# Kernel tuning notes

Hardware: AMD Instinct MI355X
Metric: run time of the kernel (lower is better)

## Reference

```python
import jax, jax.numpy as jnp
import numpy as np

QUERY_BREADTH = 50


def setup_inputs() -> dict:
    key = jax.random.key(0)
    k1, k2, k3 = jax.random.split(key, 3)
    B, D_K, D_V, M = 8192, 128, 128, 32768
    return {
        "queries": jax.random.normal(k1, (B, D_K), dtype=jnp.float32),
        "keys": jax.random.normal(k2, (M, D_K), dtype=jnp.float32),
        "values": jax.random.normal(k3, (M, D_V), dtype=jnp.float32),
    }


def reference(queries, keys, values):
    # [B, M] dense similarity (dot-product) lookup
    lookup = jnp.einsum("bd,md->bm", queries, keys)
    # top-k over memory slots
    top_ks, top_k_inds = jax.lax.top_k(lookup, QUERY_BREADTH)  # [B, K]
    weights = jax.nn.softmax(top_ks, axis=1)                   # [B, K]
    # gather value rows and weighted-sum: [B, K, D_V] -> [B, D_V]
    selected_values = values[top_k_inds]
    weighted_selection = jnp.einsum("bkd,bk->bd", selected_values, weights)
    return (weighted_selection, top_k_inds, weights)
```

## Files before the change

### kernel.cpp

```cpp
#include <hip/hip_runtime.h>
#include <hip/hip_bf16.h>

constexpr int D    = 128;
constexpr int KSEL = 50;
constexpr int CAP  = 256;
constexpr int CNT_STRIDE = 16;
constexpr int HT_PER_BLK = 16;
constexpr int SLOTS = 24;
constexpr float THR_SIGMA = 2.6f;

typedef __attribute__((ext_vector_type(8))) short bf16x8;
typedef __attribute__((ext_vector_type(4))) float f32x4;

__device__ inline unsigned short f32_to_bf16_rne(float f) {
    unsigned u = __float_as_uint(f);
    unsigned r = 0x7FFFu + ((u >> 16) & 1u);
    return (unsigned short)((u + r) >> 16);
}

#define GLOAD_LDS16(gp, lp) \
  __builtin_amdgcn_global_load_lds((const __attribute__((address_space(1))) void*)(gp), \
                                   (__attribute__((address_space(3))) void*)(lp), 16, 0, 0)

__global__ void k_convert(const float* __restrict__ src,
                          unsigned short* __restrict__ dst, int nrows) {
    int gid = blockIdx.x * 256 + threadIdx.x;
    if (gid >= nrows * 32) return;
    int r  = gid >> 5;
    int d4 = (gid & 31) << 2;
    const float4 v = *(const float4*)(src + (size_t)r * D + d4);
    ushort4 o;
    o.x = f32_to_bf16_rne(v.x);
    o.y = f32_to_bf16_rne(v.y);
    o.z = f32_to_bf16_rne(v.z);
    o.w = f32_to_bf16_rne(v.w);
    size_t base = (size_t)(r >> 6) * 8192 + (size_t)(d4 >> 3) * 512
                + (size_t)(r & 63) * 8 + (d4 & 7);
    *(ushort4*)(dst + base) = o;
}

__global__ void k0_norm(const float* __restrict__ Q, float* __restrict__ tq) {
    const int q = blockIdx.x;
    const int lane = threadIdx.x;
    float v0 = Q[(size_t)q * D + lane];
    float v1 = Q[(size_t)q * D + 64 + lane];
    float ss = v0 * v0 + v1 * v1;
    #pragma unroll
    for (int off = 32; off > 0; off >>= 1)
        ss += __shfl_xor(ss, off);
    if (lane == 0) tq[q] = THR_SIGMA * sqrtf(ss);
}

__global__ __launch_bounds__(256, 3) void k1_mfma_filter(
    const unsigned short* __restrict__ Qb, const unsigned short* __restrict__ Kb,
    const float* __restrict__ tq, int* __restrict__ cnt,
    unsigned* __restrict__ ckey)
{
    __shared__ unsigned short Ks[2][8192];
    __shared__ unsigned cand[128][SLOTS];
    __shared__ int lcnt[128];

    const int tid  = threadIdx.x;
    const int wid  = tid >> 6;
    const int lane = tid & 63;
    const int qb   = blockIdx.x;
    const int ch   = blockIdx.y;

    if (tid < 128) lcnt[tid] = 0;

    const int wq  = wid >> 1;
    const int wk  = wid & 1;
    const int fr  = lane & 15;
    const int dgl = lane >> 4;

    const unsigned short* gkc = Kb + (size_t)ch * (HT_PER_BLK * 8192);
    #pragma unroll
    for (int i = 0; i < 4; ++i) {
        int inst = wid * 4 + i;
        GLOAD_LDS16(gkc + inst * 512 + lane * 8, &Ks[0][inst * 512]);
    }

    bf16x8 qf[4][4];
    {
        const unsigned short* qbase_p = Qb + (size_t)(qb * 2 + wq) * 8192;
        #pragma unroll
        for (int ks = 0; ks < 4; ++ks)
            #pragma unroll
            for (int fi = 0; fi < 4; ++fi)
                qf[ks][fi] = *(const bf16x8*)(qbase_p + (ks * 4 + dgl) * 512
                                              + (fi * 16 + fr) * 8);
    }

    const int qbase = qb * 128 + wq * 64;
    const int crow  = (lane >> 4) * 4;
    const int ccol  = lane & 15;

    float thr[4][4];
    #pragma unroll
    for (int fi = 0; fi < 4; ++fi)
        #pragma unroll
        for (int r = 0; r < 4; ++r)
            thr[fi][r] = tq[qbase + fi * 16 + crow + r];

    __syncthreads();

    for (int t = 0; t < HT_PER_BLK; ++t) {
        const int cur = t & 1;

        if (t + 1 < HT_PER_BLK) {
            const unsigned short* gt = gkc + (size_t)(t + 1) * 8192;
            #pragma unroll
            for (int i = 0; i < 4; ++i) {
                int inst = wid * 4 + i;
                GLOAD_LDS16(gt + inst * 512 + lane * 8, &Ks[cur ^ 1][inst * 512]);
            }
        }
        __builtin_amdgcn_sched_barrier(0);

        f32x4 acc[4][2];
        const f32x4 fzero = {0.f, 0.f, 0.f, 0.f};
        #pragma unroll
        for (int i = 0; i < 4; ++i) {
            acc[i][0] = fzero; acc[i][1] = fzero;
        }

        #pragma unroll
        for (int ks = 0; ks < 4; ++ks) {
            const int dg = ks * 4 + dgl;
            bf16x8 b[2];
            #pragma unroll
            for (int fj = 0; fj < 2; ++fj)
                b[fj] = *(const bf16x8*)&Ks[cur][dg * 512
                                                + (wk * 32 + fj * 16 + fr) * 8];
            #pragma unroll
            for (int fi = 0; fi < 4; ++fi)
                #pragma unroll
                for (int fj = 0; fj < 2; ++fj)
                    acc[fi][fj] = __builtin_amdgcn_mfma_f32_16x16x32_bf16(
                        qf[ks][fi], b[fj], acc[fi][fj], 0, 0, 0);
        }

        const int kbase = (ch * HT_PER_BLK + t) * 64 + wk * 32;
        #pragma unroll
        for (int fi = 0; fi < 4; ++fi) {
            #pragma unroll
            for (int r = 0; r < 4; ++r) {
                unsigned m = 0;
                #pragma unroll
                for (int fj = 0; fj < 2; ++fj)
                    if (acc[fi][fj][r] > thr[fi][r]) m |= (1u << fj);
                if (m) {
                    const int ql = wq * 64 + fi * 16 + crow + r;
                    int p = atomicAdd(&lcnt[ql], __popc(m));
                    #pragma unroll
                    for (int fj = 0; fj < 2; ++fj) {
                        if ((m >> fj) & 1u) {
                            const int key = kbase + fj * 16 + ccol;
                            const unsigned pk =
                                ((unsigned)f32_to_bf16_rne(acc[fi][fj][r]) << 15)
                                | (unsigned)(0x7FFF - key);
                            if (p < SLOTS) cand[ql][p] = pk;
                            ++p;
                        }
                    }
                }
            }
        }
        __syncthreads();
    }

    if (tid < 128) {
        const int q = qb * 128 + tid;
        int n = lcnt[tid]; if (n > SLOTS) n = SLOTS;
        if (n > 0) {
            int base = atomicAdd(&cnt[(size_t)q * CNT_STRIDE], n);
            for (int i = 0; i < n; ++i) {
                int p = base + i;
                if (p < CAP) ckey[(size_t)q * CAP + p] = cand[tid][i];
            }
        }
    }
}

__global__ __launch_bounds__(256) void k2_select(
    const float* __restrict__ Q, const float* __restrict__ Kmat,
    const float* __restrict__ V,
    const unsigned* __restrict__ ckey, const int* __restrict__ cnt, int M,
    float* __restrict__ outW, float* __restrict__ outI, float* __restrict__ outP)
{
    const int lane = threadIdx.x & 63;
    const int wid  = threadIdx.x >> 6;
    const int q    = blockIdx.x * 4 + wid;

    __shared__ float Qrow[4][D];
    Qrow[wid][lane]      = Q[(size_t)q * D + lane];
    Qrow[wid][lane + 64] = Q[(size_t)q * D + lane + 64];
    __syncthreads();

    int n = cnt[(size_t)q * CNT_STRIDE]; if (n > CAP) n = CAP;

    unsigned key[4];
    #pragma unroll
    for (int s = 0; s < 4; ++s) {
        int pos = s * 64 + lane;
        key[s] = (pos < n) ? ckey[(size_t)q * CAP + pos] : 0u;
    }

    #pragma unroll
    for (int k = 2; k <= 256; k <<= 1) {
        #pragma unroll
        for (int j = k >> 1; j > 0; j >>= 1) {
            if (j >= 64) {
                const int jr = j >> 6;
                #pragma unroll
                for (int r = 0; r < 4; ++r) {
                    if ((r & jr) == 0) {
                        const int r2 = r | jr;
                        const bool up = (((r << 6) & k) == 0);
                        const bool sw = up ? (key[r2] > key[r]) : (key[r2] < key[r]);
                        if (sw) { unsigned tmp = key[r]; key[r] = key[r2]; key[r2] = tmp; }
                    }
                }
            } else {
                #pragma unroll
                for (int r = 0; r < 4; ++r) {
                    unsigned other = __shfl_xor(key[r], j);
                    const bool up = ((((r << 6) | lane) & k) == 0);
                    const bool hi = (lane & j) != 0;
                    const bool oBetter = other > key[r];
                    const bool keepOther = (up != hi) ? oBetter : !oBetter;
                    if (keepOther) key[r] = other;
                }
            }
        }
    }

    const unsigned key0 = key[0];
    const int id0 = key0 ? (0x7FFF - (int)(key0 & 0x7FFFu)) : 0x7FFFFFFF;

    float sv;
    {
        const float* kr = Kmat + (size_t)(key0 ? id0 : 0) * D;
        float a = 0.f;
        #pragma unroll 8
        for (int d0 = 0; d0 < D; d0 += 4) {
            float4 kv = *(const float4*)(kr + d0);
            a = fmaf(Qrow[wid][d0 + 0], kv.x, a);
            a = fmaf(Qrow[wid][d0 + 1], kv.y, a);
            a = fmaf(Qrow[wid][d0 + 2], kv.z, a);
            a = fmaf(Qrow[wid][d0 + 3], kv.w, a);
        }
        sv = key0 ? a : -__builtin_inff();
    }

    unsigned long long fk = key0
        ? (((unsigned long long)__float_as_uint(sv) << 32)
           | (unsigned long long)(0xFFFFFFFFu - (unsigned)id0))
        : 0ull;
    #pragma unroll
    for (int k = 2; k <= 64; k <<= 1) {
        #pragma unroll
        for (int j = k >> 1; j > 0; j >>= 1) {
            unsigned long long other = __shfl_xor(fk, j);
            const bool up = ((lane & k) == 0) || (k == 64);
            const bool hi = (lane & j) != 0;
            const bool oBetter = other > fk;
            const bool keepOther = (up != hi) ? oBetter : !oBetter;
            if (keepOther) fk = other;
        }
    }
    float svf = __uint_as_float((unsigned)(fk >> 32));
    int   si  = (int)(0xFFFFFFFFu - (unsigned)(fk & 0xFFFFFFFFull));

    float m0 = __shfl(svf, 0);
    float e = (lane < KSEL) ? (float)exp((double)svf - (double)m0) : 0.f;
    float sum = e;
    #pragma unroll
    for (int off = 32; off > 0; off >>= 1) sum += __shfl_xor(sum, off);
    float w = e / sum;

    if (lane < KSEL) {
        outI[(size_t)q * KSEL + lane] = (float)si;
        outP[(size_t)q * KSEL + lane] = w;
    }

    float g0 = 0.f, g1 = 0.f;
    for (int cc = 0; cc < KSEL; ++cc) {
        int   idc = __shfl(si, cc);
        float wc  = __shfl(w,  cc);
        if ((unsigned)idc >= (unsigned)M) idc = 0;
        const float2 vv = *(const float2*)(V + (size_t)idc * D + lane * 2);
        g0 = fmaf(wc, vv.x, g0);
        g1 = fmaf(wc, vv.y, g1);
    }
    float2 res; res.x = g0; res.y = g1;
    *(float2*)(outW + (size_t)q * D + lane * 2) = res;
}

extern "C" void kernel_launch(void* const* d_in, const int* in_sizes, int n_in,
                              void* d_out, int out_size, void* d_ws, size_t ws_size,
                              hipStream_t stream) {
    const float* Q  = (const float*)d_in[0];
    const float* Km = (const float*)d_in[1];
    const float* V  = (const float*)d_in[2];

    const int B = in_sizes[0] / D;
    const int M = in_sizes[1] / D;

    float* out  = (float*)d_out;
    float* outW = out;
    float* outI = out + (size_t)B * D;
    float* outP = outI + (size_t)B * KSEL;

    char* ws = (char*)d_ws;
    float*          tq   = (float*)ws;
    int*            cnt  = (int*)(ws + (size_t)B * 4);
    unsigned*       ckey = (unsigned*)(ws + (size_t)B * 4 + (size_t)B * CNT_STRIDE * 4);
    unsigned short* Qb   = (unsigned short*)((char*)ckey + (size_t)B * CAP * 4);
    unsigned short* Kb   = (unsigned short*)((char*)Qb + (size_t)B * D * 2);

    hipMemsetAsync(cnt, 0, (size_t)B * CNT_STRIDE * 4, stream);
    k_convert<<<(B * 32 + 255) / 256, 256, 0, stream>>>(Q,  Qb, B);
    k_convert<<<(M * 32 + 255) / 256, 256, 0, stream>>>(Km, Kb, M);
    k0_norm<<<B, 64, 0, stream>>>(Q, tq);
    dim3 g1(B / 128, M / (64 * HT_PER_BLK));
    k1_mfma_filter<<<g1, 256, 0, stream>>>(Qb, Kb, tq, cnt, ckey);
    k2_select<<<B / 4, 256, 0, stream>>>(Q, Km, V, ckey, cnt, M, outW, outI, outP);
}
```

Measured before the change: 202.4 us.

## Load key tiles straight to registers and fuse query norm into conversion

The filter kernel no longer stages key tiles through double-buffered LDS with async global-to-LDS loads. Each wave now reads its B fragments directly from global memory (L2-cached), which removes the per-tile barrier and the 32KB LDS buffer. The query-norm threshold is computed inside the bf16 conversion kernel, so the separate norm launch goes away, and the occupancy hint in launch bounds is dropped. The trade-off is that every wave issues redundant global loads for the same keys, with no software prefetch to hide latency.

```diff
diff --git a/kernel.cpp b/kernel.cpp
--- a/kernel.cpp
+++ b/kernel.cpp
@@ -5,7 +5,7 @@
 constexpr int KSEL = 50;
 constexpr int CAP  = 256;
 constexpr int CNT_STRIDE = 16;
-constexpr int HT_PER_BLK = 16;
+constexpr int GRP_PER_BLK = 16;
 constexpr int SLOTS = 24;
 constexpr float THR_SIGMA = 2.6f;
 
@@ -18,17 +18,21 @@
     return (unsigned short)((u + r) >> 16);
 }
 
-#define GLOAD_LDS16(gp, lp) \
-  __builtin_amdgcn_global_load_lds((const __attribute__((address_space(1))) void*)(gp), \
-                                   (__attribute__((address_space(3))) void*)(lp), 16, 0, 0)
-
 __global__ void k_convert(const float* __restrict__ src,
-                          unsigned short* __restrict__ dst, int nrows) {
+                          unsigned short* __restrict__ dst, int nrows,
+                          float* __restrict__ tq) {
     int gid = blockIdx.x * 256 + threadIdx.x;
     if (gid >= nrows * 32) return;
     int r  = gid >> 5;
     int d4 = (gid & 31) << 2;
     const float4 v = *(const float4*)(src + (size_t)r * D + d4);
+    if (tq) {
+        float ss = v.x * v.x + v.y * v.y + v.z * v.z + v.w * v.w;
+        #pragma unroll
+        for (int off = 16; off > 0; off >>= 1)
+            ss += __shfl_xor(ss, off);
+        if ((gid & 31) == 0) tq[r] = THR_SIGMA * sqrtf(ss);
+    }
     ushort4 o;
     o.x = f32_to_bf16_rne(v.x);
     o.y = f32_to_bf16_rne(v.y);
@@ -39,24 +43,11 @@
     *(ushort4*)(dst + base) = o;
 }
 
-__global__ void k0_norm(const float* __restrict__ Q, float* __restrict__ tq) {
-    const int q = blockIdx.x;
-    const int lane = threadIdx.x;
-    float v0 = Q[(size_t)q * D + lane];
-    float v1 = Q[(size_t)q * D + 64 + lane];
-    float ss = v0 * v0 + v1 * v1;
-    #pragma unroll
-    for (int off = 32; off > 0; off >>= 1)
-        ss += __shfl_xor(ss, off);
-    if (lane == 0) tq[q] = THR_SIGMA * sqrtf(ss);
-}
-
-__global__ __launch_bounds__(256, 3) void k1_mfma_filter(
+__global__ __launch_bounds__(256) void k1_mfma_filter(
     const unsigned short* __restrict__ Qb, const unsigned short* __restrict__ Kb,
     const float* __restrict__ tq, int* __restrict__ cnt,
     unsigned* __restrict__ ckey)
 {
-    __shared__ unsigned short Ks[2][8192];
     __shared__ unsigned cand[128][SLOTS];
     __shared__ int lcnt[128];
 
@@ -73,21 +64,14 @@
     const int fr  = lane & 15;
     const int dgl = lane >> 4;
 
-    const unsigned short* gkc = Kb + (size_t)ch * (HT_PER_BLK * 8192);
-    #pragma unroll
-    for (int i = 0; i < 4; ++i) {
-        int inst = wid * 4 + i;
-        GLOAD_LDS16(gkc + inst * 512 + lane * 8, &Ks[0][inst * 512]);
-    }
-
     bf16x8 qf[4][4];
     {
-        const unsigned short* qbase_p = Qb + (size_t)(qb * 2 + wq) * 8192;
+        const unsigned short* qp = Qb + (size_t)(qb * 2 + wq) * 8192;
         #pragma unroll
         for (int ks = 0; ks < 4; ++ks)
             #pragma unroll
             for (int fi = 0; fi < 4; ++fi)
-                qf[ks][fi] = *(const bf16x8*)(qbase_p + (ks * 4 + dgl) * 512
+                qf[ks][fi] = *(const bf16x8*)(qp + (ks * 4 + dgl) * 512
                                               + (fi * 16 + fr) * 8);
     }
 
@@ -104,43 +88,32 @@
 
     __syncthreads();
 
-    for (int t = 0; t < HT_PER_BLK; ++t) {
-        const int cur = t & 1;
-
-        if (t + 1 < HT_PER_BLK) {
-            const unsigned short* gt = gkc + (size_t)(t + 1) * 8192;
+    for (int g = 0; g < GRP_PER_BLK; ++g) {
+        const unsigned short* gp = Kb + (size_t)(ch * GRP_PER_BLK + g) * 8192;
+
+        bf16x8 b[4][2];
+        #pragma unroll
+        for (int ks = 0; ks < 4; ++ks)
             #pragma unroll
-            for (int i = 0; i < 4; ++i) {
-                int inst = wid * 4 + i;
-                GLOAD_LDS16(gt + inst * 512 + lane * 8, &Ks[cur ^ 1][inst * 512]);
-            }
-        }
-        __builtin_amdgcn_sched_barrier(0);
+            for (int fj = 0; fj < 2; ++fj)
+                b[ks][fj] = *(const bf16x8*)(gp + (ks * 4 + dgl) * 512
+                                             + (wk * 32 + fj * 16 + fr) * 8);
 
         f32x4 acc[4][2];
         const f32x4 fzero = {0.f, 0.f, 0.f, 0.f};
         #pragma unroll
-        for (int i = 0; i < 4; ++i) {
-            acc[i][0] = fzero; acc[i][1] = fzero;
-        }
-
-        #pragma unroll
-        for (int ks = 0; ks < 4; ++ks) {
-            const int dg = ks * 4 + dgl;
-            bf16x8 b[2];
-            #pragma unroll
-            for (int fj = 0; fj < 2; ++fj)
-                b[fj] = *(const bf16x8*)&Ks[cur][dg * 512
-                                                + (wk * 32 + fj * 16 + fr) * 8];
+        for (int i = 0; i < 4; ++i) { acc[i][0] = fzero; acc[i][1] = fzero; }
+
+        #pragma unroll
+        for (int ks = 0; ks < 4; ++ks)
             #pragma unroll
             for (int fi = 0; fi < 4; ++fi)
                 #pragma unroll
                 for (int fj = 0; fj < 2; ++fj)
                     acc[fi][fj] = __builtin_amdgcn_mfma_f32_16x16x32_bf16(
-                        qf[ks][fi], b[fj], acc[fi][fj], 0, 0, 0);
-        }
-
-        const int kbase = (ch * HT_PER_BLK + t) * 64 + wk * 32;
+                        qf[ks][fi], b[ks][fj], acc[fi][fj], 0, 0, 0);
+
+        const int kbase = (ch * GRP_PER_BLK + g) * 64 + wk * 32;
         #pragma unroll
         for (int fi = 0; fi < 4; ++fi) {
             #pragma unroll
@@ -166,8 +139,9 @@
                 }
             }
         }
-        __syncthreads();
-    }
+    }
+
+    __syncthreads();
 
     if (tid < 128) {
         const int q = qb * 128 + tid;
@@ -320,10 +294,9 @@
     unsigned short* Kb   = (unsigned short*)((char*)Qb + (size_t)B * D * 2);
 
     hipMemsetAsync(cnt, 0, (size_t)B * CNT_STRIDE * 4, stream);
-    k_convert<<<(B * 32 + 255) / 256, 256, 0, stream>>>(Q,  Qb, B);
-    k_convert<<<(M * 32 + 255) / 256, 256, 0, stream>>>(Km, Kb, M);
-    k0_norm<<<B, 64, 0, stream>>>(Q, tq);
-    dim3 g1(B / 128, M / (64 * HT_PER_BLK));
+    k_convert<<<(B * 32 + 255) / 256, 256, 0, stream>>>(Q,  Qb, B, tq);
+    k_convert<<<(M * 32 + 255) / 256, 256, 0, stream>>>(Km, Kb, M, nullptr);
+    dim3 g1(B / 128, M / (64 * GRP_PER_BLK));
     k1_mfma_filter<<<g1, 256, 0, stream>>>(Qb, Kb, tq, cnt, ckey);
     k2_select<<<B / 4, 256, 0, stream>>>(Q, Km, V, ckey, cnt, M, outW, outI, outP);
 }
```

Measured after the change: 204.5 us. About the same (+1.0%).
